# Kernel tuning notes

Hardware: AMD Instinct MI355X
Metric: run time of the kernel (lower is better)

The kernel has to match this reference:

```python
import jax, jax.numpy as jnp
import numpy as np

N = 50000      # nodes
E = 800000     # edges (avg degree 16)
D_IN, D_H, D_OUT = 128, 128, 64


def setup_inputs() -> dict:
    key = jax.random.key(0)
    ks = jax.random.split(key, 12)
    s = 0.05  # weight init scale
    return {
        "x": jax.random.normal(ks[0], (N, D_IN), jnp.float32),
        "edge_index": jax.random.randint(ks[1], (2, E), 0, N, dtype=jnp.int64),
        "Wl0": jax.random.normal(ks[2], (D_H, D_IN), jnp.float32) * s,
        "bl0": jax.random.normal(ks[3], (D_H,), jnp.float32) * s,
        "Wr0": jax.random.normal(ks[4], (D_H, D_IN), jnp.float32) * s,
        "Wl1": jax.random.normal(ks[5], (D_H, D_H), jnp.float32) * s,
        "bl1": jax.random.normal(ks[6], (D_H,), jnp.float32) * s,
        "Wr1": jax.random.normal(ks[7], (D_H, D_H), jnp.float32) * s,
        "Wl2": jax.random.normal(ks[8], (D_OUT, D_H), jnp.float32) * s,
        "bl2": jax.random.normal(ks[9], (D_OUT,), jnp.float32) * s,
        "Wr2": jax.random.normal(ks[10], (D_OUT, D_H), jnp.float32) * s,
    }


def _sage_layer(h, src, dst, Wl, bl, Wr):
    # mean aggregation over incoming neighbors: out[i] = mean_{j in N(i)} h[j]
    n = h.shape[0]
    agg = jax.ops.segment_sum(h[src], dst, num_segments=n)          # [N, D]
    deg = jax.ops.segment_sum(jnp.ones((src.shape[0],), h.dtype), dst,
                              num_segments=n)                        # [N]
    mean = agg / jnp.maximum(deg, 1.0)[:, None]  # empty rows -> 0, matches torch_sparse
    # lin_l(agg) + lin_r(self); lin_r has no bias in PyG SAGEConv
    return mean @ Wl.T + bl + h @ Wr.T


def reference(x, edge_index, Wl0, bl0, Wr0, Wl1, bl1, Wr1, Wl2, bl2, Wr2):
    src, dst = edge_index[1], edge_index[0]  # adj row = dst, col = src
    h = jax.nn.relu(_sage_layer(x, src, dst, Wl0, bl0, Wr0))
    h = jax.nn.relu(_sage_layer(h, src, dst, Wl1, bl1, Wr1))
    h = _sage_layer(h, src, dst, Wl2, bl2, Wr2)
    return jax.nn.log_softmax(h, axis=1)
```

## Files before the change

kernel.cpp:

```cpp
#include <hip/hip_runtime.h>
#include <hip/hip_bf16.h>


typedef __attribute__((ext_vector_type(8))) short bf16x8;
typedef __attribute__((ext_vector_type(4))) float f32x4;

#define NPB 128
#define BCAP 2560
#define EPB 8192
#define EPT 32
#define CPAD 16

__device__ __forceinline__ unsigned short f2bf(float f) {
    unsigned int u = __builtin_bit_cast(unsigned int, f);
    u += 0x7fffu + ((u >> 16) & 1u);
    return (unsigned short)(u >> 16);
}
__device__ __forceinline__ float bf2f(unsigned int bits16) {
    return __builtin_bit_cast(float, bits16 << 16);
}


__global__ __launch_bounds__(256) void distribute_kernel(const int* __restrict__ dst,
                                                         const int* __restrict__ srcv,
                                                         int* __restrict__ gcnt,
                                                         unsigned int* __restrict__ staging,
                                                         int E, int NBc) {
    __shared__ unsigned int stage[EPB];
    __shared__ int hist[400];
    __shared__ int lstart[400];
    __shared__ int gbase[400];
    __shared__ int scanbuf[256];
    int t = threadIdx.x;
    int e0 = blockIdx.x * EPB;
    unsigned int w[EPT];

    for (int b = t; b < NBc + 1; b += 256) hist[b] = 0;
    __syncthreads();

#pragma unroll
    for (int i = 0; i < EPT; ++i) {
        int e = e0 + i * 256 + t;
        unsigned int word = 0xFFFFFFFFu;
        if (e < E) word = ((unsigned int)dst[e] << 16) | (unsigned int)srcv[e];
        w[i] = word;
        int b = (int)(word >> 23); if (b > NBc) b = NBc;
        atomicAdd(&hist[b], 1);
    }
    __syncthreads();

    int b0 = 2 * t, b1 = 2 * t + 1;
    int h0 = (b0 <= NBc) ? hist[b0] : 0;
    int h1 = (b1 <= NBc) ? hist[b1] : 0;
    int pair = h0 + h1;
    scanbuf[t] = pair;
    __syncthreads();
    for (int off = 1; off < 256; off <<= 1) {
        int v = (t >= off) ? scanbuf[t - off] : 0;
        __syncthreads();
        scanbuf[t] += v;
        __syncthreads();
    }
    int excl = scanbuf[t] - pair;
    if (b0 <= NBc) lstart[b0] = excl;
    if (b1 <= NBc) lstart[b1] = excl + h0;
    __syncthreads();

    for (int b = t; b < NBc; b += 256) {
        int h = hist[b];
        gbase[b] = h ? atomicAdd(&gcnt[b * CPAD], h) : 0;
    }
    for (int b = t; b < NBc + 1; b += 256) hist[b] = lstart[b];
    __syncthreads();

#pragma unroll
    for (int i = 0; i < EPT; ++i) {
        unsigned int word = w[i];
        int b = (int)(word >> 23); if (b > NBc) b = NBc;
        int p = atomicAdd(&hist[b], 1);
        stage[p] = word;
    }
    __syncthreads();

    int total = lstart[NBc];
    for (int i = t; i < total; i += 256) {
        unsigned int word = stage[i];
        int b = (int)(word >> 23);
        int gpos = gbase[b] + (i - lstart[b]);
        staging[(size_t)b * BCAP + gpos] = word;
    }
}


__global__ __launch_bounds__(512) void bucket_scan_kernel(const int* __restrict__ gcnt,
                                                          int* __restrict__ base, int NBc,
                                                          int* __restrict__ rowptr_last) {
    __shared__ int sh[512];
    int t = threadIdx.x;
    int v = (t < NBc) ? gcnt[t * CPAD] : 0;
    sh[t] = v; __syncthreads();
    for (int off = 1; off < 512; off <<= 1) {
        int u = (t >= off) ? sh[t - off] : 0;
        __syncthreads();
        sh[t] += u;
        __syncthreads();
    }
    if (t < NBc) base[t] = sh[t] - v;
    if (t == 511) *rowptr_last = sh[511];
}


__global__ __launch_bounds__(256) void build_kernel(const unsigned int* __restrict__ staging,
                                                    const int* __restrict__ gcnt,
                                                    const int* __restrict__ base,
                                                    int* __restrict__ row_ptr,
                                                    int* __restrict__ adj, int N) {
    __shared__ int hist[NPB];
    __shared__ int scn[NPB];
    int b = blockIdx.x;
    int t = threadIdx.x;
    int n0 = b * NPB;
    int nb = N - n0; if (nb > NPB) nb = NPB;
    int ec = gcnt[b * CPAD];
    int bb = base[b];
    const unsigned int* st = staging + (size_t)b * BCAP;

    if (t < NPB) hist[t] = 0;
    __syncthreads();
    for (int i = t; i < ec; i += 256)
        atomicAdd(&hist[(st[i] >> 16) & (NPB - 1)], 1);
    __syncthreads();

    int v = (t < NPB) ? hist[t] : 0;
    if (t < NPB) scn[t] = v;
    __syncthreads();
    for (int off = 1; off < NPB; off <<= 1) {
        int u = (t >= off && t < NPB) ? scn[t - off] : 0;
        __syncthreads();
        if (t < NPB) scn[t] += u;
        __syncthreads();
    }
    if (t < NPB) hist[t] = scn[t] - v;
    if (t < nb) row_ptr[n0 + t] = bb + (scn[t] - v);
    __syncthreads();

    for (int i = t; i < ec; i += 256) {
        unsigned int pk = st[i];
        int p = atomicAdd(&hist[(pk >> 16) & (NPB - 1)], 1);
        adj[bb + p] = (int)(pk & 0xffffu);
    }
}


__global__ void cast_all_kernel(const float* __restrict__ x,
                                const float* p0, const float* p1, const float* p2,
                                const float* p3, const float* p4, const float* p5,
                                unsigned short* __restrict__ xbf,
                                unsigned short* __restrict__ wbf, int xpairs) {
    int bid = blockIdx.x;
    int xblocks = (xpairs + 255) / 256;
    if (bid < xblocks) {
        int i = bid * 256 + threadIdx.x;
        if (i < xpairs) {
            float2 v = ((const float2*)x)[i];
            unsigned int p = (unsigned int)f2bf(v.x) | ((unsigned int)f2bf(v.y) << 16);
            ((unsigned int*)xbf)[i] = p;
        }
    } else {
        int w = (bid - xblocks) * 256 + threadIdx.x;
        if (w < 40960) {
            const float* src;
            int local;
            if      (w < 8192)  { src = p0; local = w; }
            else if (w < 16384) { src = p1; local = w - 8192; }
            else if (w < 24576) { src = p2; local = w - 16384; }
            else if (w < 32768) { src = p3; local = w - 24576; }
            else if (w < 36864) { src = p4; local = w - 32768; }
            else                { src = p5; local = w - 36864; }
            float2 v = ((const float2*)src)[local];
            unsigned int p = (unsigned int)f2bf(v.x) | ((unsigned int)f2bf(v.y) << 16);
            ((unsigned int*)wbf)[w] = p;
        }
    }
}


__global__ __launch_bounds__(256) void gemm_mfma_kernel(const unsigned short* __restrict__ H,
                                                        const unsigned short* __restrict__ Wl,
                                                        const unsigned short* __restrict__ Wr,
                                                        unsigned short* __restrict__ C,
                                                        int N, int ldC) {
    int wave = threadIdx.x >> 6;
    int lane = threadIdx.x & 63;
    int l15 = lane & 15, quad = lane >> 4;
    int y = blockIdx.y, half = gridDim.y >> 1;
    const unsigned short* W = (y < half) ? Wl : Wr;
    int wrow0 = (y < half ? y : y - half) * 64;
    int col0 = y * 64;
    int m0 = blockIdx.x * 128 + wave * 32;

    int r0 = m0 + l15;      if (r0 > N - 1) r0 = N - 1;
    int r1 = m0 + 16 + l15; if (r1 > N - 1) r1 = N - 1;
    const bf16x8* A0 = (const bf16x8*)(H + (size_t)r0 * 128);
    const bf16x8* A1 = (const bf16x8*)(H + (size_t)r1 * 128);

    f32x4 acc[2][4] = {};
#pragma unroll
    for (int ks = 0; ks < 4; ++ks) {
        int vidx = ks * 4 + quad;
        bf16x8 a0 = A0[vidx];
        bf16x8 a1 = A1[vidx];
#pragma unroll
        for (int j = 0; j < 4; ++j) {
            const bf16x8* B = (const bf16x8*)(W + (size_t)(wrow0 + j * 16 + l15) * 128);
            bf16x8 b = B[vidx];
            acc[0][j] = __builtin_amdgcn_mfma_f32_16x16x32_bf16(a0, b, acc[0][j], 0, 0, 0);
            acc[1][j] = __builtin_amdgcn_mfma_f32_16x16x32_bf16(a1, b, acc[1][j], 0, 0, 0);
        }
    }

#pragma unroll
    for (int i = 0; i < 2; ++i)
#pragma unroll
        for (int j = 0; j < 4; ++j)
#pragma unroll
            for (int r = 0; r < 4; ++r) {
                int row = m0 + i * 16 + quad * 4 + r;
                if (row < N) {
                    int col = col0 + j * 16 + l15;
                    C[(size_t)row * ldC + col] = f2bf(acc[i][j][r]);
                }
            }
}


__global__ __launch_bounds__(256) void agg_relu_kernel(const unsigned short* __restrict__ C,
                                                       const int* __restrict__ row_ptr,
                                                       const int* __restrict__ adj,
                                                       const float* __restrict__ bias,
                                                       unsigned short* __restrict__ hout, int N) {
    int node = (int)((blockIdx.x * blockDim.x + threadIdx.x) >> 6);
    int lane = threadIdx.x & 63;
    if (node >= N) return;
    int beg = row_ptr[node], end = row_ptr[node + 1];
    float sx0 = 0.f, sy0 = 0.f, sx1 = 0.f, sy1 = 0.f;
    float sx2 = 0.f, sy2 = 0.f, sx3 = 0.f, sy3 = 0.f;

    int e = beg;
    while (e < end) {
        int cnt = end - e; if (cnt > 64) cnt = 64;
        int ll = lane; if (ll > cnt - 1) ll = cnt - 1;
        int myidx = adj[e + ll];

        int i = 0;
        for (; i + 8 <= cnt; i += 8) {
            int s0 = __shfl(myidx, i + 0), s1 = __shfl(myidx, i + 1);
            int s2 = __shfl(myidx, i + 2), s3 = __shfl(myidx, i + 3);
            int s4 = __shfl(myidx, i + 4), s5 = __shfl(myidx, i + 5);
            int s6 = __shfl(myidx, i + 6), s7 = __shfl(myidx, i + 7);
            unsigned int v0 = ((const unsigned int*)(C + (size_t)s0 * 256))[lane];
            unsigned int v1 = ((const unsigned int*)(C + (size_t)s1 * 256))[lane];
            unsigned int v2 = ((const unsigned int*)(C + (size_t)s2 * 256))[lane];
            unsigned int v3 = ((const unsigned int*)(C + (size_t)s3 * 256))[lane];
            unsigned int v4 = ((const unsigned int*)(C + (size_t)s4 * 256))[lane];
            unsigned int v5 = ((const unsigned int*)(C + (size_t)s5 * 256))[lane];
            unsigned int v6 = ((const unsigned int*)(C + (size_t)s6 * 256))[lane];
            unsigned int v7 = ((const unsigned int*)(C + (size_t)s7 * 256))[lane];
            sx0 += bf2f(v0 & 0xffffu); sy0 += bf2f(v0 >> 16);
            sx1 += bf2f(v1 & 0xffffu); sy1 += bf2f(v1 >> 16);
            sx2 += bf2f(v2 & 0xffffu); sy2 += bf2f(v2 >> 16);
            sx3 += bf2f(v3 & 0xffffu); sy3 += bf2f(v3 >> 16);
            sx0 += bf2f(v4 & 0xffffu); sy0 += bf2f(v4 >> 16);
            sx1 += bf2f(v5 & 0xffffu); sy1 += bf2f(v5 >> 16);
            sx2 += bf2f(v6 & 0xffffu); sy2 += bf2f(v6 >> 16);
            sx3 += bf2f(v7 & 0xffffu); sy3 += bf2f(v7 >> 16);
        }
        if (i < cnt) {
            int rem = cnt - i, c1 = cnt - 1;
            int t0 = i, t1 = i + 1, t2 = i + 2, t3 = i + 3;
            int t4 = i + 4, t5 = i + 5, t6 = i + 6, t7 = i + 7;
            int s0 = __shfl(myidx, t0 > c1 ? c1 : t0), s1 = __shfl(myidx, t1 > c1 ? c1 : t1);
            int s2 = __shfl(myidx, t2 > c1 ? c1 : t2), s3 = __shfl(myidx, t3 > c1 ? c1 : t3);
            int s4 = __shfl(myidx, t4 > c1 ? c1 : t4), s5 = __shfl(myidx, t5 > c1 ? c1 : t5);
            int s6 = __shfl(myidx, t6 > c1 ? c1 : t6), s7 = __shfl(myidx, t7 > c1 ? c1 : t7);
            unsigned int v0 = ((const unsigned int*)(C + (size_t)s0 * 256))[lane];
            unsigned int v1 = ((const unsigned int*)(C + (size_t)s1 * 256))[lane];
            unsigned int v2 = ((const unsigned int*)(C + (size_t)s2 * 256))[lane];
            unsigned int v3 = ((const unsigned int*)(C + (size_t)s3 * 256))[lane];
            unsigned int v4 = ((const unsigned int*)(C + (size_t)s4 * 256))[lane];
            unsigned int v5 = ((const unsigned int*)(C + (size_t)s5 * 256))[lane];
            unsigned int v6 = ((const unsigned int*)(C + (size_t)s6 * 256))[lane];
            unsigned int v7 = ((const unsigned int*)(C + (size_t)s7 * 256))[lane];
            float m1 = rem > 1 ? 1.f : 0.f, m2 = rem > 2 ? 1.f : 0.f, m3 = rem > 3 ? 1.f : 0.f;
            float m4 = rem > 4 ? 1.f : 0.f, m5 = rem > 5 ? 1.f : 0.f, m6 = rem > 6 ? 1.f : 0.f;
            float m7 = rem > 7 ? 1.f : 0.f;
            sx0 += bf2f(v0 & 0xffffu);      sy0 += bf2f(v0 >> 16);
            sx1 += m1 * bf2f(v1 & 0xffffu); sy1 += m1 * bf2f(v1 >> 16);
            sx2 += m2 * bf2f(v2 & 0xffffu); sy2 += m2 * bf2f(v2 >> 16);
            sx3 += m3 * bf2f(v3 & 0xffffu); sy3 += m3 * bf2f(v3 >> 16);
            sx0 += m4 * bf2f(v4 & 0xffffu); sy0 += m4 * bf2f(v4 >> 16);
            sx1 += m5 * bf2f(v5 & 0xffffu); sy1 += m5 * bf2f(v5 >> 16);
            sx2 += m6 * bf2f(v6 & 0xffffu); sy2 += m6 * bf2f(v6 >> 16);
            sx3 += m7 * bf2f(v7 & 0xffffu); sy3 += m7 * bf2f(v7 >> 16);
        }
        e += cnt;
    }

    float sx = (sx0 + sx1) + (sx2 + sx3);
    float sy = (sy0 + sy1) + (sy2 + sy3);
    int deg = end - beg;
    float inv = 1.0f / (float)(deg > 1 ? deg : 1);
    float2 bb = ((const float2*)bias)[lane];
    unsigned int rv = ((const unsigned int*)(C + (size_t)node * 256))[64 + lane];
    float ox = fmaxf(sx * inv + bb.x + bf2f(rv & 0xffffu), 0.f);
    float oy = fmaxf(sy * inv + bb.y + bf2f(rv >> 16), 0.f);
    unsigned int p = (unsigned int)f2bf(ox) | ((unsigned int)f2bf(oy) << 16);
    ((unsigned int*)(hout + (size_t)node * 128))[lane] = p;
}


__global__ __launch_bounds__(256) void final_kernel(const unsigned short* __restrict__ C,
                                                    const int* __restrict__ row_ptr,
                                                    const int* __restrict__ adj,
                                                    const float* __restrict__ bias,
                                                    float* __restrict__ out, int N) {
    int node = (int)((blockIdx.x * blockDim.x + threadIdx.x) >> 6);
    int lane = threadIdx.x & 63;
    if (node >= N) return;
    int beg = row_ptr[node], end = row_ptr[node + 1];
    float a0 = 0.f, a1 = 0.f, a2 = 0.f, a3 = 0.f;

    int e = beg;
    while (e < end) {
        int cnt = end - e; if (cnt > 64) cnt = 64;
        int ll = lane; if (ll > cnt - 1) ll = cnt - 1;
        int myidx = adj[e + ll];

        int i = 0;
        for (; i + 8 <= cnt; i += 8) {
            int s0 = __shfl(myidx, i + 0), s1 = __shfl(myidx, i + 1);
            int s2 = __shfl(myidx, i + 2), s3 = __shfl(myidx, i + 3);
            int s4 = __shfl(myidx, i + 4), s5 = __shfl(myidx, i + 5);
            int s6 = __shfl(myidx, i + 6), s7 = __shfl(myidx, i + 7);
            float v0 = bf2f((unsigned int)C[(size_t)s0 * 128 + lane]);
            float v1 = bf2f((unsigned int)C[(size_t)s1 * 128 + lane]);
            float v2 = bf2f((unsigned int)C[(size_t)s2 * 128 + lane]);
            float v3 = bf2f((unsigned int)C[(size_t)s3 * 128 + lane]);
            float v4 = bf2f((unsigned int)C[(size_t)s4 * 128 + lane]);
            float v5 = bf2f((unsigned int)C[(size_t)s5 * 128 + lane]);
            float v6 = bf2f((unsigned int)C[(size_t)s6 * 128 + lane]);
            float v7 = bf2f((unsigned int)C[(size_t)s7 * 128 + lane]);
            a0 += v0 + v4; a1 += v1 + v5; a2 += v2 + v6; a3 += v3 + v7;
        }
        if (i < cnt) {
            int rem = cnt - i, c1 = cnt - 1;
            int t;
            t = i + 0; int s0 = __shfl(myidx, t > c1 ? c1 : t);
            t = i + 1; int s1 = __shfl(myidx, t > c1 ? c1 : t);
            t = i + 2; int s2 = __shfl(myidx, t > c1 ? c1 : t);
            t = i + 3; int s3 = __shfl(myidx, t > c1 ? c1 : t);
            t = i + 4; int s4 = __shfl(myidx, t > c1 ? c1 : t);
            t = i + 5; int s5 = __shfl(myidx, t > c1 ? c1 : t);
            t = i + 6; int s6 = __shfl(myidx, t > c1 ? c1 : t);
            t = i + 7; int s7 = __shfl(myidx, t > c1 ? c1 : t);
            float v0 = bf2f((unsigned int)C[(size_t)s0 * 128 + lane]);
            float v1 = bf2f((unsigned int)C[(size_t)s1 * 128 + lane]);
            float v2 = bf2f((unsigned int)C[(size_t)s2 * 128 + lane]);
            float v3 = bf2f((unsigned int)C[(size_t)s3 * 128 + lane]);
            float v4 = bf2f((unsigned int)C[(size_t)s4 * 128 + lane]);
            float v5 = bf2f((unsigned int)C[(size_t)s5 * 128 + lane]);
            float v6 = bf2f((unsigned int)C[(size_t)s6 * 128 + lane]);
            float v7 = bf2f((unsigned int)C[(size_t)s7 * 128 + lane]);
            float m1 = rem > 1 ? 1.f : 0.f, m2 = rem > 2 ? 1.f : 0.f, m3 = rem > 3 ? 1.f : 0.f;
            float m4 = rem > 4 ? 1.f : 0.f, m5 = rem > 5 ? 1.f : 0.f, m6 = rem > 6 ? 1.f : 0.f;
            float m7 = rem > 7 ? 1.f : 0.f;
            a0 += v0 + m4 * v4; a1 += m1 * v1 + m5 * v5;
            a2 += m2 * v2 + m6 * v6; a3 += m3 * v3 + m7 * v7;
        }
        e += cnt;
    }

    float sum = (a0 + a1) + (a2 + a3);
    int deg = end - beg;
    float inv = 1.0f / (float)(deg > 1 ? deg : 1);
    float u = sum * inv + bias[lane] + bf2f((unsigned int)C[(size_t)node * 128 + 64 + lane]);

    float m = u;
#pragma unroll
    for (int off = 32; off > 0; off >>= 1) m = fmaxf(m, __shfl_xor(m, off));
    float ex = __expf(u - m);
    float se = ex;
#pragma unroll
    for (int off = 32; off > 0; off >>= 1) se += __shfl_xor(se, off);
    out[(size_t)node * 64 + lane] = (u - m) - __logf(se);
}


extern "C" void kernel_launch(void* const* d_in, const int* in_sizes, int n_in,
                              void* d_out, int out_size, void* d_ws, size_t ws_size,
                              hipStream_t stream) {
    const float* x   = (const float*)d_in[0];
    const int*   ei  = (const int*)d_in[1];
    const float* Wl0 = (const float*)d_in[2];
    const float* bl0 = (const float*)d_in[3];
    const float* Wr0 = (const float*)d_in[4];
    const float* Wl1 = (const float*)d_in[5];
    const float* bl1 = (const float*)d_in[6];
    const float* Wr1 = (const float*)d_in[7];
    const float* Wl2 = (const float*)d_in[8];
    const float* bl2 = (const float*)d_in[9];
    const float* Wr2 = (const float*)d_in[10];
    float* out = (float*)d_out;

    const int N  = in_sizes[0] / 128;
    const int E  = in_sizes[1] / 2;
    const int NB = (N + NPB - 1) / NPB;

    char* ws = (char*)d_ws;
    auto alloc = [&](size_t bytes) {
        char* p = ws;
        ws += (bytes + 255) & ~(size_t)255;
        return p;
    };
    int*   row_ptr    = (int*)alloc((size_t)(N + 1) * 4);
    int*   adj        = (int*)alloc((size_t)E * 4);
    int*   gcnt       = (int*)alloc((size_t)NB * CPAD * 4);
    int*   bucketBase = (int*)alloc((size_t)NB * 4);
    unsigned int* staging = (unsigned int*)alloc((size_t)NB * BCAP * 4);
    unsigned short* xbf = (unsigned short*)alloc((size_t)N * 128 * 2);
    unsigned short* wbf = (unsigned short*)alloc((size_t)81920 * 2);
    unsigned short* C   = (unsigned short*)alloc((size_t)N * 256 * 2);
    unsigned short* hA  = (unsigned short*)alloc((size_t)N * 128 * 2);
    unsigned short* hB  = (unsigned short*)alloc((size_t)N * 128 * 2);

    const int* dstp = ei;
    const int* srcp = ei + E;

    hipMemsetAsync(gcnt, 0, (size_t)NB * CPAD * 4, stream);
    int distBlocks = (E + EPB - 1) / EPB;
    distribute_kernel<<<distBlocks, 256, 0, stream>>>(dstp, srcp, gcnt, staging, E, NB);
    bucket_scan_kernel<<<1, 512, 0, stream>>>(gcnt, bucketBase, NB, row_ptr + N);
    build_kernel<<<NB, 256, 0, stream>>>(staging, gcnt, bucketBase, row_ptr, adj, N);

    int xpairs = N * 64;
    int castBlocks = (xpairs + 255) / 256 + 160;
    cast_all_kernel<<<castBlocks, 256, 0, stream>>>(x, Wl0, Wr0, Wl1, Wr1, Wl2, Wr2,
                                                    xbf, wbf, xpairs);
    unsigned short* wl0 = wbf;
    unsigned short* wr0 = wbf + 16384;
    unsigned short* wl1 = wbf + 32768;
    unsigned short* wr1 = wbf + 49152;
    unsigned short* wl2 = wbf + 65536;
    unsigned short* wr2 = wbf + 73728;

    dim3 blk(256);
    int gemmRows = (N + 127) / 128;
    int aggBlocks = (N * 64 + 255) / 256;

    gemm_mfma_kernel<<<dim3(gemmRows, 4), blk, 0, stream>>>(xbf, wl0, wr0, C, N, 256);
    agg_relu_kernel<<<aggBlocks, blk, 0, stream>>>(C, row_ptr, adj, bl0, hA, N);
    gemm_mfma_kernel<<<dim3(gemmRows, 4), blk, 0, stream>>>(hA, wl1, wr1, C, N, 256);
    agg_relu_kernel<<<aggBlocks, blk, 0, stream>>>(C, row_ptr, adj, bl1, hB, N);
    gemm_mfma_kernel<<<dim3(gemmRows, 2), blk, 0, stream>>>(hB, wl2, wr2, C, N, 128);
    final_kernel<<<aggBlocks, blk, 0, stream>>>(C, row_ptr, adj, bl2, out, N);
}
```

Before: 276.0 us.

## Fuse cast into distribute kernel, fold bucket scan into build, widen gather unroll

After: 281.5 us. Within noise of the previous version (+2.0%).

```diff
diff --git a/kernel.cpp b/kernel.cpp
--- a/kernel.cpp
+++ b/kernel.cpp
@@ -21,17 +21,50 @@
 }
 
 
-__global__ __launch_bounds__(256) void distribute_kernel(const int* __restrict__ dst,
-                                                         const int* __restrict__ srcv,
-                                                         int* __restrict__ gcnt,
-                                                         unsigned int* __restrict__ staging,
-                                                         int E, int NBc) {
+__global__ __launch_bounds__(256) void dist_cast_kernel(
+        const int* __restrict__ dst, const int* __restrict__ srcv,
+        int* __restrict__ gcnt, unsigned int* __restrict__ staging, int E, int NBc,
+        const float* __restrict__ x,
+        const float* p0, const float* p1, const float* p2,
+        const float* p3, const float* p4, const float* p5,
+        unsigned short* __restrict__ xbf, unsigned short* __restrict__ wbf,
+        int xpairs, int distBlocks) {
     __shared__ unsigned int stage[EPB];
     __shared__ int hist[400];
     __shared__ int lstart[400];
     __shared__ int gbase[400];
     __shared__ int scanbuf[256];
     int t = threadIdx.x;
+
+    if (blockIdx.x >= distBlocks) {
+        int bid = blockIdx.x - distBlocks;
+        int xblocks = (xpairs + 255) / 256;
+        if (bid < xblocks) {
+            int i = bid * 256 + t;
+            if (i < xpairs) {
+                float2 v = ((const float2*)x)[i];
+                unsigned int p = (unsigned int)f2bf(v.x) | ((unsigned int)f2bf(v.y) << 16);
+                ((unsigned int*)xbf)[i] = p;
+            }
+        } else {
+            int w = (bid - xblocks) * 256 + t;
+            if (w < 40960) {
+                const float* src;
+                int local;
+                if      (w < 8192)  { src = p0; local = w; }
+                else if (w < 16384) { src = p1; local = w - 8192; }
+                else if (w < 24576) { src = p2; local = w - 16384; }
+                else if (w < 32768) { src = p3; local = w - 24576; }
+                else if (w < 36864) { src = p4; local = w - 32768; }
+                else                { src = p5; local = w - 36864; }
+                float2 v = ((const float2*)src)[local];
+                unsigned int p = (unsigned int)f2bf(v.x) | ((unsigned int)f2bf(v.y) << 16);
+                ((unsigned int*)wbf)[w] = p;
+            }
+        }
+        return;
+    }
+
     int e0 = blockIdx.x * EPB;
     unsigned int w[EPT];
 
@@ -92,37 +125,39 @@
 }
 
 
-__global__ __launch_bounds__(512) void bucket_scan_kernel(const int* __restrict__ gcnt,
-                                                          int* __restrict__ base, int NBc,
-                                                          int* __restrict__ rowptr_last) {
-    __shared__ int sh[512];
-    int t = threadIdx.x;
-    int v = (t < NBc) ? gcnt[t * CPAD] : 0;
-    sh[t] = v; __syncthreads();
-    for (int off = 1; off < 512; off <<= 1) {
-        int u = (t >= off) ? sh[t - off] : 0;
-        __syncthreads();
-        sh[t] += u;
-        __syncthreads();
-    }
-    if (t < NBc) base[t] = sh[t] - v;
-    if (t == 511) *rowptr_last = sh[511];
-}
-
-
 __global__ __launch_bounds__(256) void build_kernel(const unsigned int* __restrict__ staging,
                                                     const int* __restrict__ gcnt,
-                                                    const int* __restrict__ base,
                                                     int* __restrict__ row_ptr,
-                                                    int* __restrict__ adj, int N) {
+                                                    int* __restrict__ adj, int N, int NBc) {
+    __shared__ int lstart[400];
+    __shared__ int scanbuf[256];
     __shared__ int hist[NPB];
     __shared__ int scn[NPB];
     int b = blockIdx.x;
     int t = threadIdx.x;
+
+    int b0 = 2 * t, b1 = 2 * t + 1;
+    int h0 = (b0 < NBc) ? gcnt[b0 * CPAD] : 0;
+    int h1 = (b1 < NBc) ? gcnt[b1 * CPAD] : 0;
+    int pair = h0 + h1;
+    scanbuf[t] = pair;
+    __syncthreads();
+    for (int off = 1; off < 256; off <<= 1) {
+        int v = (t >= off) ? scanbuf[t - off] : 0;
+        __syncthreads();
+        scanbuf[t] += v;
+        __syncthreads();
+    }
+    int excl = scanbuf[t] - pair;
+    if (b0 < NBc) lstart[b0] = excl;
+    if (b1 < NBc) lstart[b1] = excl + h0;
+    if (b == 0 && t == 255) row_ptr[N] = scanbuf[255];
+    __syncthreads();
+
     int n0 = b * NPB;
     int nb = N - n0; if (nb > NPB) nb = NPB;
     int ec = gcnt[b * CPAD];
-    int bb = base[b];
+    int bb = lstart[b];
     const unsigned int* st = staging + (size_t)b * BCAP;
 
     if (t < NPB) hist[t] = 0;
@@ -148,39 +183,6 @@
         unsigned int pk = st[i];
         int p = atomicAdd(&hist[(pk >> 16) & (NPB - 1)], 1);
         adj[bb + p] = (int)(pk & 0xffffu);
-    }
-}
-
-
-__global__ void cast_all_kernel(const float* __restrict__ x,
-                                const float* p0, const float* p1, const float* p2,
-                                const float* p3, const float* p4, const float* p5,
-                                unsigned short* __restrict__ xbf,
-                                unsigned short* __restrict__ wbf, int xpairs) {
-    int bid = blockIdx.x;
-    int xblocks = (xpairs + 255) / 256;
-    if (bid < xblocks) {
-        int i = bid * 256 + threadIdx.x;
-        if (i < xpairs) {
-            float2 v = ((const float2*)x)[i];
-            unsigned int p = (unsigned int)f2bf(v.x) | ((unsigned int)f2bf(v.y) << 16);
-            ((unsigned int*)xbf)[i] = p;
-        }
-    } else {
-        int w = (bid - xblocks) * 256 + threadIdx.x;
-        if (w < 40960) {
-            const float* src;
-            int local;
-            if      (w < 8192)  { src = p0; local = w; }
-            else if (w < 16384) { src = p1; local = w - 8192; }
-            else if (w < 24576) { src = p2; local = w - 16384; }
-            else if (w < 32768) { src = p3; local = w - 24576; }
-            else if (w < 36864) { src = p4; local = w - 32768; }
-            else                { src = p5; local = w - 36864; }
-            float2 v = ((const float2*)src)[local];
-            unsigned int p = (unsigned int)f2bf(v.x) | ((unsigned int)f2bf(v.y) << 16);
-            ((unsigned int*)wbf)[w] = p;
-        }
     }
 }
 
@@ -243,77 +245,42 @@
     int lane = threadIdx.x & 63;
     if (node >= N) return;
     int beg = row_ptr[node], end = row_ptr[node + 1];
-    float sx0 = 0.f, sy0 = 0.f, sx1 = 0.f, sy1 = 0.f;
-    float sx2 = 0.f, sy2 = 0.f, sx3 = 0.f, sy3 = 0.f;
+    float sx[4] = {}, sy[4] = {};
 
     int e = beg;
     while (e < end) {
         int cnt = end - e; if (cnt > 64) cnt = 64;
-        int ll = lane; if (ll > cnt - 1) ll = cnt - 1;
+        int c1 = cnt - 1;
+        int ll = lane > c1 ? c1 : lane;
         int myidx = adj[e + ll];
 
-        int i = 0;
-        for (; i + 8 <= cnt; i += 8) {
-            int s0 = __shfl(myidx, i + 0), s1 = __shfl(myidx, i + 1);
-            int s2 = __shfl(myidx, i + 2), s3 = __shfl(myidx, i + 3);
-            int s4 = __shfl(myidx, i + 4), s5 = __shfl(myidx, i + 5);
-            int s6 = __shfl(myidx, i + 6), s7 = __shfl(myidx, i + 7);
-            unsigned int v0 = ((const unsigned int*)(C + (size_t)s0 * 256))[lane];
-            unsigned int v1 = ((const unsigned int*)(C + (size_t)s1 * 256))[lane];
-            unsigned int v2 = ((const unsigned int*)(C + (size_t)s2 * 256))[lane];
-            unsigned int v3 = ((const unsigned int*)(C + (size_t)s3 * 256))[lane];
-            unsigned int v4 = ((const unsigned int*)(C + (size_t)s4 * 256))[lane];
-            unsigned int v5 = ((const unsigned int*)(C + (size_t)s5 * 256))[lane];
-            unsigned int v6 = ((const unsigned int*)(C + (size_t)s6 * 256))[lane];
-            unsigned int v7 = ((const unsigned int*)(C + (size_t)s7 * 256))[lane];
-            sx0 += bf2f(v0 & 0xffffu); sy0 += bf2f(v0 >> 16);
-            sx1 += bf2f(v1 & 0xffffu); sy1 += bf2f(v1 >> 16);
-            sx2 += bf2f(v2 & 0xffffu); sy2 += bf2f(v2 >> 16);
-            sx3 += bf2f(v3 & 0xffffu); sy3 += bf2f(v3 >> 16);
-            sx0 += bf2f(v4 & 0xffffu); sy0 += bf2f(v4 >> 16);
-            sx1 += bf2f(v5 & 0xffffu); sy1 += bf2f(v5 >> 16);
-            sx2 += bf2f(v6 & 0xffffu); sy2 += bf2f(v6 >> 16);
-            sx3 += bf2f(v7 & 0xffffu); sy3 += bf2f(v7 >> 16);
-        }
-        if (i < cnt) {
-            int rem = cnt - i, c1 = cnt - 1;
-            int t0 = i, t1 = i + 1, t2 = i + 2, t3 = i + 3;
-            int t4 = i + 4, t5 = i + 5, t6 = i + 6, t7 = i + 7;
-            int s0 = __shfl(myidx, t0 > c1 ? c1 : t0), s1 = __shfl(myidx, t1 > c1 ? c1 : t1);
-            int s2 = __shfl(myidx, t2 > c1 ? c1 : t2), s3 = __shfl(myidx, t3 > c1 ? c1 : t3);
-            int s4 = __shfl(myidx, t4 > c1 ? c1 : t4), s5 = __shfl(myidx, t5 > c1 ? c1 : t5);
-            int s6 = __shfl(myidx, t6 > c1 ? c1 : t6), s7 = __shfl(myidx, t7 > c1 ? c1 : t7);
-            unsigned int v0 = ((const unsigned int*)(C + (size_t)s0 * 256))[lane];
-            unsigned int v1 = ((const unsigned int*)(C + (size_t)s1 * 256))[lane];
-            unsigned int v2 = ((const unsigned int*)(C + (size_t)s2 * 256))[lane];
-            unsigned int v3 = ((const unsigned int*)(C + (size_t)s3 * 256))[lane];
-            unsigned int v4 = ((const unsigned int*)(C + (size_t)s4 * 256))[lane];
-            unsigned int v5 = ((const unsigned int*)(C + (size_t)s5 * 256))[lane];
-            unsigned int v6 = ((const unsigned int*)(C + (size_t)s6 * 256))[lane];
-            unsigned int v7 = ((const unsigned int*)(C + (size_t)s7 * 256))[lane];
-            float m1 = rem > 1 ? 1.f : 0.f, m2 = rem > 2 ? 1.f : 0.f, m3 = rem > 3 ? 1.f : 0.f;
-            float m4 = rem > 4 ? 1.f : 0.f, m5 = rem > 5 ? 1.f : 0.f, m6 = rem > 6 ? 1.f : 0.f;
-            float m7 = rem > 7 ? 1.f : 0.f;
-            sx0 += bf2f(v0 & 0xffffu);      sy0 += bf2f(v0 >> 16);
-            sx1 += m1 * bf2f(v1 & 0xffffu); sy1 += m1 * bf2f(v1 >> 16);
-            sx2 += m2 * bf2f(v2 & 0xffffu); sy2 += m2 * bf2f(v2 >> 16);
-            sx3 += m3 * bf2f(v3 & 0xffffu); sy3 += m3 * bf2f(v3 >> 16);
-            sx0 += m4 * bf2f(v4 & 0xffffu); sy0 += m4 * bf2f(v4 >> 16);
-            sx1 += m5 * bf2f(v5 & 0xffffu); sy1 += m5 * bf2f(v5 >> 16);
-            sx2 += m6 * bf2f(v6 & 0xffffu); sy2 += m6 * bf2f(v6 >> 16);
-            sx3 += m7 * bf2f(v7 & 0xffffu); sy3 += m7 * bf2f(v7 >> 16);
+        for (int i = 0; i < cnt; i += 16) {
+            int rem = cnt - i;
+            unsigned int v[16];
+#pragma unroll
+            for (int j = 0; j < 16; ++j) {
+                int tt = i + j; if (tt > c1) tt = c1;
+                int s = __shfl(myidx, tt);
+                v[j] = ((const unsigned int*)(C + (size_t)s * 256))[lane];
+            }
+#pragma unroll
+            for (int j = 0; j < 16; ++j) {
+                float m = (j < rem) ? 1.f : 0.f;
+                sx[j & 3] += m * bf2f(v[j] & 0xffffu);
+                sy[j & 3] += m * bf2f(v[j] >> 16);
+            }
         }
         e += cnt;
     }
 
-    float sx = (sx0 + sx1) + (sx2 + sx3);
-    float sy = (sy0 + sy1) + (sy2 + sy3);
+    float fx = (sx[0] + sx[1]) + (sx[2] + sx[3]);
+    float fy = (sy[0] + sy[1]) + (sy[2] + sy[3]);
     int deg = end - beg;
     float inv = 1.0f / (float)(deg > 1 ? deg : 1);
     float2 bb = ((const float2*)bias)[lane];
     unsigned int rv = ((const unsigned int*)(C + (size_t)node * 256))[64 + lane];
-    float ox = fmaxf(sx * inv + bb.x + bf2f(rv & 0xffffu), 0.f);
-    float oy = fmaxf(sy * inv + bb.y + bf2f(rv >> 16), 0.f);
+    float ox = fmaxf(fx * inv + bb.x + bf2f(rv & 0xffffu), 0.f);
+    float oy = fmaxf(fy * inv + bb.y + bf2f(rv >> 16), 0.f);
     unsigned int p = (unsigned int)f2bf(ox) | ((unsigned int)f2bf(oy) << 16);
     ((unsigned int*)(hout + (size_t)node * 128))[lane] = p;
 }
@@ -328,59 +295,34 @@
     int lane = threadIdx.x & 63;
     if (node >= N) return;
     int beg = row_ptr[node], end = row_ptr[node + 1];
-    float a0 = 0.f, a1 = 0.f, a2 = 0.f, a3 = 0.f;
+    float a[4] = {};
 
     int e = beg;
     while (e < end) {
         int cnt = end - e; if (cnt > 64) cnt = 64;
-        int ll = lane; if (ll > cnt - 1) ll = cnt - 1;
+        int c1 = cnt - 1;
+        int ll = lane > c1 ? c1 : lane;
         int myidx = adj[e + ll];
 
-        int i = 0;
-        for (; i + 8 <= cnt; i += 8) {
-            int s0 = __shfl(myidx, i + 0), s1 = __shfl(myidx, i + 1);
-            int s2 = __shfl(myidx, i + 2), s3 = __shfl(myidx, i + 3);
-            int s4 = __shfl(myidx, i + 4), s5 = __shfl(myidx, i + 5);
-            int s6 = __shfl(myidx, i + 6), s7 = __shfl(myidx, i + 7);
-            float v0 = bf2f((unsigned int)C[(size_t)s0 * 128 + lane]);
-            float v1 = bf2f((unsigned int)C[(size_t)s1 * 128 + lane]);
-            float v2 = bf2f((unsigned int)C[(size_t)s2 * 128 + lane]);
-            float v3 = bf2f((unsigned int)C[(size_t)s3 * 128 + lane]);
-            float v4 = bf2f((unsigned int)C[(size_t)s4 * 128 + lane]);
-            float v5 = bf2f((unsigned int)C[(size_t)s5 * 128 + lane]);
-            float v6 = bf2f((unsigned int)C[(size_t)s6 * 128 + lane]);
-            float v7 = bf2f((unsigned int)C[(size_t)s7 * 128 + lane]);
-            a0 += v0 + v4; a1 += v1 + v5; a2 += v2 + v6; a3 += v3 + v7;
-        }
-        if (i < cnt) {
-            int rem = cnt - i, c1 = cnt - 1;
-            int t;
-            t = i + 0; int s0 = __shfl(myidx, t > c1 ? c1 : t);
-            t = i + 1; int s1 = __shfl(myidx, t > c1 ? c1 : t);
-            t = i + 2; int s2 = __shfl(myidx, t > c1 ? c1 : t);
-            t = i + 3; int s3 = __shfl(myidx, t > c1 ? c1 : t);
-            t = i + 4; int s4 = __shfl(myidx, t > c1 ? c1 : t);
-            t = i + 5; int s5 = __shfl(myidx, t > c1 ? c1 : t);
-            t = i + 6; int s6 = __shfl(myidx, t > c1 ? c1 : t);
-            t = i + 7; int s7 = __shfl(myidx, t > c1 ? c1 : t);
-            float v0 = bf2f((unsigned int)C[(size_t)s0 * 128 + lane]);
-            float v1 = bf2f((unsigned int)C[(size_t)s1 * 128 + lane]);
-            float v2 = bf2f((unsigned int)C[(size_t)s2 * 128 + lane]);
-            float v3 = bf2f((unsigned int)C[(size_t)s3 * 128 + lane]);
-            float v4 = bf2f((unsigned int)C[(size_t)s4 * 128 + lane]);
-            float v5 = bf2f((unsigned int)C[(size_t)s5 * 128 + lane]);
-            float v6 = bf2f((unsigned int)C[(size_t)s6 * 128 + lane]);
-            float v7 = bf2f((unsigned int)C[(size_t)s7 * 128 + lane]);
-            float m1 = rem > 1 ? 1.f : 0.f, m2 = rem > 2 ? 1.f : 0.f, m3 = rem > 3 ? 1.f : 0.f;
-            float m4 = rem > 4 ? 1.f : 0.f, m5 = rem > 5 ? 1.f : 0.f, m6 = rem > 6 ? 1.f : 0.f;
-            float m7 = rem > 7 ? 1.f : 0.f;
-            a0 += v0 + m4 * v4; a1 += m1 * v1 + m5 * v5;
-            a2 += m2 * v2 + m6 * v6; a3 += m3 * v3 + m7 * v7;
+        for (int i = 0; i < cnt; i += 16) {
+            int rem = cnt - i;
+            float v[16];
+#pragma unroll
+            for (int j = 0; j < 16; ++j) {
+                int tt = i + j; if (tt > c1) tt = c1;
+                int s = __shfl(myidx, tt);
+                v[j] = bf2f((unsigned int)C[(size_t)s * 128 + lane]);
+            }
+#pragma unroll
+            for (int j = 0; j < 16; ++j) {
+                float m = (j < rem) ? 1.f : 0.f;
+                a[j & 3] += m * v[j];
+            }
         }
         e += cnt;
     }
 
-    float sum = (a0 + a1) + (a2 + a3);
+    float sum = (a[0] + a[1]) + (a[2] + a[3]);
     int deg = end - beg;
     float inv = 1.0f / (float)(deg > 1 ? deg : 1);
     float u = sum * inv + bias[lane] + bf2f((unsigned int)C[(size_t)node * 128 + 64 + lane]);
@@ -422,10 +364,9 @@
         ws += (bytes + 255) & ~(size_t)255;
         return p;
     };
-    int*   row_ptr    = (int*)alloc((size_t)(N + 1) * 4);
-    int*   adj        = (int*)alloc((size_t)E * 4);
-    int*   gcnt       = (int*)alloc((size_t)NB * CPAD * 4);
-    int*   bucketBase = (int*)alloc((size_t)NB * 4);
+    int*   row_ptr = (int*)alloc((size_t)(N + 1) * 4);
+    int*   adj     = (int*)alloc((size_t)E * 4);
+    int*   gcnt    = (int*)alloc((size_t)NB * CPAD * 4);
     unsigned int* staging = (unsigned int*)alloc((size_t)NB * BCAP * 4);
     unsigned short* xbf = (unsigned short*)alloc((size_t)N * 128 * 2);
     unsigned short* wbf = (unsigned short*)alloc((size_t)81920 * 2);
@@ -437,15 +378,16 @@
     const int* srcp = ei + E;
 
     hipMemsetAsync(gcnt, 0, (size_t)NB * CPAD * 4, stream);
+
     int distBlocks = (E + EPB - 1) / EPB;
-    distribute_kernel<<<distBlocks, 256, 0, stream>>>(dstp, srcp, gcnt, staging, E, NB);
-    bucket_scan_kernel<<<1, 512, 0, stream>>>(gcnt, bucketBase, NB, row_ptr + N);
-    build_kernel<<<NB, 256, 0, stream>>>(staging, gcnt, bucketBase, row_ptr, adj, N);
-
     int xpairs = N * 64;
     int castBlocks = (xpairs + 255) / 256 + 160;
-    cast_all_kernel<<<castBlocks, 256, 0, stream>>>(x, Wl0, Wr0, Wl1, Wr1, Wl2, Wr2,
-                                                    xbf, wbf, xpairs);
+    dist_cast_kernel<<<distBlocks + castBlocks, 256, 0, stream>>>(
+        dstp, srcp, gcnt, staging, E, NB,
+        x, Wl0, Wr0, Wl1, Wr1, Wl2, Wr2, xbf, wbf, xpairs, distBlocks);
+
+    build_kernel<<<NB, 256, 0, stream>>>(staging, gcnt, row_ptr, adj, N, NB);
+
     unsigned short* wl0 = wbf;
     unsigned short* wr0 = wbf + 16384;
     unsigned short* wl1 = wbf + 32768;
```
